# Performance work log

Hardware: AMD Instinct MI355X
Metric: run time of the kernel (lower is better)

The kernel has to match this reference:

```python
import jax, jax.numpy as jnp
import numpy as np

K = 5          # number of spline bins
B = 5.0        # tail bound
HIDDEN = 8
MIN_W = 1e-3; MIN_H = 1e-3; MIN_D = 1e-3  # RQS defaults (Durkan et al.)


def setup_inputs() -> dict:
    n, d = 32768, 64
    L = d - 1
    P = 3 * K - 1
    ks = jax.random.split(jax.random.key(0), 8)
    x = jax.random.normal(ks[0], (n, d), jnp.float32) * 2.0
    init_param = jax.random.uniform(ks[1], (P,), jnp.float32, -0.5, 0.5)
    # ragged first layers: layer l (predicts dim l+1) sees x[:, :l+1]; zero-pad to width L
    mask = (jnp.arange(L)[None, :] <= jnp.arange(L)[:, None]).astype(jnp.float32)
    W1 = jax.random.normal(ks[2], (L, L, HIDDEN), jnp.float32) * 0.2 * mask[:, :, None]
    b1 = jax.random.normal(ks[3], (L, HIDDEN), jnp.float32) * 0.1
    W2 = jax.random.normal(ks[4], (L, HIDDEN, HIDDEN), jnp.float32) * 0.2
    b2 = jax.random.normal(ks[5], (L, HIDDEN), jnp.float32) * 0.1
    W3 = jax.random.normal(ks[6], (L, HIDDEN, P), jnp.float32) * 0.2
    b3 = jax.random.normal(ks[7], (L, P), jnp.float32) * 0.1
    return {"x": x, "init_param": init_param, "W1": W1, "b1": b1,
            "W2": W2, "b2": b2, "W3": W3, "b3": b3}


def _rqs(xf, Wu, Hu, Du):
    # xf: (M,), Wu/Hu: (M,K), Du: (M,K-1) -- vectorized unconstrained RQS, forward
    inside = (xf >= -B) & (xf <= B)
    const = float(np.log(np.exp(1.0 - MIN_D) - 1.0))
    Dpad = jnp.pad(Du, ((0, 0), (1, 1)), constant_values=const)

    widths = MIN_W + (1.0 - MIN_W * K) * jax.nn.softmax(Wu, axis=-1)
    cumw = jnp.pad(jnp.cumsum(widths, -1), ((0, 0), (1, 0)))
    cumw = 2.0 * B * cumw - B
    cumw = cumw.at[:, 0].set(-B).at[:, -1].set(B)
    widths = cumw[:, 1:] - cumw[:, :-1]

    heights = MIN_H + (1.0 - MIN_H * K) * jax.nn.softmax(Hu, axis=-1)
    cumh = jnp.pad(jnp.cumsum(heights, -1), ((0, 0), (1, 0)))
    cumh = 2.0 * B * cumh - B
    cumh = cumh.at[:, 0].set(-B).at[:, -1].set(B)
    heights = cumh[:, 1:] - cumh[:, :-1]

    derivs = MIN_D + jax.nn.softplus(Dpad)  # (M, K+1)

    xc = jnp.clip(xf, -B, B)
    idx = jnp.clip(jnp.sum(xc[:, None] >= cumw, axis=-1) - 1, 0, K - 1)
    take = lambda a: jnp.take_along_axis(a, idx[:, None], axis=-1)[:, 0]

    icw, ibw = take(cumw), take(widths)
    ich, ih = take(cumh), take(heights)
    idl = take(heights / widths)
    idv = take(derivs)
    idvp1 = take(derivs[:, 1:])

    theta = (xc - icw) / ibw
    tmt = theta * (1.0 - theta)
    num = ih * (idl * theta * theta + idv * tmt)
    den = idl + (idv + idvp1 - 2.0 * idl) * tmt
    out = ich + num / den
    dnum = idl * idl * (idvp1 * theta * theta + 2.0 * idl * tmt + idv * (1.0 - theta) ** 2)
    ld = jnp.log(dnum) - 2.0 * jnp.log(den)
    return jnp.where(inside, out, xf), jnp.where(inside, ld, 0.0)


def reference(x, init_param, W1, b1, W2, b2, W3, b3):
    n, d = x.shape
    L = d - 1
    P = 3 * K - 1
    # mask re-applied so padded W1 entries are exactly inert (ragged Linear(i, hidden))
    mask = (jnp.arange(L)[None, :] <= jnp.arange(L)[:, None]).astype(x.dtype)
    h = jnp.tanh(jnp.einsum('nj,ljh->lnh', x[:, :L], W1 * mask[:, :, None]) + b1[:, None, :])
    h = jnp.tanh(jnp.einsum('lnh,lhg->lng', h, W2) + b2[:, None, :])
    out = jnp.einsum('lng,lgp->lnp', h, W3) + b3[:, None, :]      # (L, n, P)
    p0 = jnp.broadcast_to(init_param, (1, n, P))                  # dim 0 uses init_param
    params = jnp.concatenate([p0, out], axis=0).reshape(d * n, P)  # dim-major, matches Ws layout
    Wu, Hu, Du = params[:, :K], params[:, K:2 * K], params[:, 2 * K:]
    xf = x.T.reshape(-1)  # x.transpose(0,1).flatten()
    zs, lds = _rqs(xf, Wu, Hu, Du)
    # NOTE: faithfully replicates the original's reshape of the dim-major flat
    # vector directly to (n, d) (as in the torch source).
    return zs.reshape(n, d), lds.reshape(n, d).sum(axis=1)
```

## Files before the change

### kernel.cpp

```cpp
#include <hip/hip_runtime.h>
#include <hip/hip_bf16.h>
#include <math.h>

#define KK 5
#define Bc 5.0f
#define NN 32768
#define DD 64
#define LL 63
#define PP 14
#define MIN_Wc 0.001f
#define MIN_Hc 0.001f
#define MIN_Dc 0.001f
#define LOG2E 1.44269504088896340736f
#define TWOLOG2E 2.88539008177792681472f
#define LN2 0.69314718055994530942f

typedef float f4 __attribute__((ext_vector_type(4)));
typedef float f32x4 __attribute__((ext_vector_type(4)));
typedef float f2 __attribute__((ext_vector_type(2)));
typedef short short8 __attribute__((ext_vector_type(8)));

__device__ __forceinline__ float rcp_fast(float v)   { return __builtin_amdgcn_rcpf(v); }
__device__ __forceinline__ float exp2_fast(float v)  { return __builtin_amdgcn_exp2f(v); }
__device__ __forceinline__ float log2_fast(float v)  { return __builtin_amdgcn_logf(v); }
__device__ __forceinline__ float tanh_pre(float t2) {
    float e = exp2_fast(t2);
    return 1.0f - 2.0f * rcp_fast(e + 1.0f);
}
__device__ __forceinline__ float softplus2(float v2) {
    return (v2 > 21.7f) ? LN2 * v2 : LN2 * log2_fast(1.0f + exp2_fast(v2));
}
__device__ __forceinline__ ushort to_bf16t(float v) {
    return (ushort)(__float_as_uint(v) >> 16);
}
__device__ __forceinline__ unsigned pack_bf16t2(float v0, float v1) {
    return (__float_as_uint(v0) >> 16) | (__float_as_uint(v1) & 0xFFFF0000u);
}
__device__ __forceinline__ float bflo(unsigned u) { return __uint_as_float(u << 16); }
__device__ __forceinline__ float bfhi(unsigned u) { return __uint_as_float(u & 0xFFFF0000u); }
__device__ __forceinline__ f2 splat2(float v) { f2 r; r.x = v; r.y = v; return r; }
__device__ __forceinline__ f4 splat4(float v) { f4 r; r.x = v; r.y = v; r.z = v; r.w = v; return r; }

__device__ __forceinline__ short8 pack_a(f4 v0, f4 v1) {
    short8 a;
    a[0] = (short)to_bf16t(v0.x); a[1] = (short)to_bf16t(v0.y);
    a[2] = (short)to_bf16t(v0.z); a[3] = (short)to_bf16t(v0.w);
    a[4] = (short)to_bf16t(v1.x); a[5] = (short)to_bf16t(v1.y);
    a[6] = (short)to_bf16t(v1.z); a[7] = (short)to_bf16t(v1.w);
    return a;
}

#define WSL 216
#define H1S 72
#define BS  72

__device__ __forceinline__ void do_dim2(
    int dd, const float* wp, float xf0, float xf1, uint4 hv0, uint4 hv1,
    int s0, int lane, int bx,
    const float* __restrict__ ip, float* __restrict__ out)
{
    float h0_0 = bflo(hv0.x), h1_0 = bflo(hv1.x);
    float h0_1 = bfhi(hv0.x), h1_1 = bfhi(hv1.x);
    float h0_2 = bflo(hv0.y), h1_2 = bflo(hv1.y);
    float h0_3 = bfhi(hv0.y), h1_3 = bfhi(hv1.y);
    float h0_4 = bflo(hv0.z), h1_4 = bflo(hv1.z);
    float h0_5 = bfhi(hv0.z), h1_5 = bfhi(hv1.z);
    float h0_6 = bflo(hv0.w), h1_6 = bflo(hv1.w);
    float h0_7 = bfhi(hv0.w), h1_7 = bfhi(hv1.w);

    f4 a0 = *(const f4*)(wp + 64), b0 = *(const f4*)(wp + 68);
    f4 a1 = a0, b1 = b0;
#define L2STEP(HI, X0, X1) { \
    f4 wa = *(const f4*)(wp + (HI) * 8); \
    f4 wb = *(const f4*)(wp + (HI) * 8 + 4); \
    f4 v0 = splat4(X0), v1 = splat4(X1); \
    a0 += v0 * wa; a1 += v1 * wa; \
    b0 += v0 * wb; b1 += v1 * wb; }
    L2STEP(0, h0_0, h1_0)
    L2STEP(1, h0_1, h1_1)
    L2STEP(2, h0_2, h1_2)
    L2STEP(3, h0_3, h1_3)
    L2STEP(4, h0_4, h1_4)
    L2STEP(5, h0_5, h1_5)
    L2STEP(6, h0_6, h1_6)
    L2STEP(7, h0_7, h1_7)
#undef L2STEP
    float g0_0 = tanh_pre(a0.x), g1_0 = tanh_pre(a1.x);
    float g0_1 = tanh_pre(a0.y), g1_1 = tanh_pre(a1.y);
    float g0_2 = tanh_pre(a0.z), g1_2 = tanh_pre(a1.z);
    float g0_3 = tanh_pre(a0.w), g1_3 = tanh_pre(a1.w);
    float g0_4 = tanh_pre(b0.x), g1_4 = tanh_pre(b1.x);
    float g0_5 = tanh_pre(b0.y), g1_5 = tanh_pre(b1.y);
    float g0_6 = tanh_pre(b0.z), g1_6 = tanh_pre(b1.z);
    float g0_7 = tanh_pre(b0.w), g1_7 = tanh_pre(b1.w);

    f4 pa0 = *(const f4*)(wp + 200), pb0 = *(const f4*)(wp + 204);
    f4 pc0 = *(const f4*)(wp + 208), pd0 = *(const f4*)(wp + 212);
    f4 pa1 = pa0, pb1 = pb0, pc1 = pc0, pd1 = pd0;
#define L3STEP(GI, X0, X1) { \
    const float* wr = wp + 72 + (GI) * 16; \
    f4 w0 = *(const f4*)(wr); \
    f4 w1 = *(const f4*)(wr + 4); \
    f4 w2 = *(const f4*)(wr + 8); \
    f4 w3 = *(const f4*)(wr + 12); \
    f4 v0 = splat4(X0), v1 = splat4(X1); \
    pa0 += v0 * w0; pa1 += v1 * w0; \
    pb0 += v0 * w1; pb1 += v1 * w1; \
    pc0 += v0 * w2; pc1 += v1 * w2; \
    pd0 += v0 * w3; pd1 += v1 * w3; }
    L3STEP(0, g0_0, g1_0)
    L3STEP(1, g0_1, g1_1)
    L3STEP(2, g0_2, g1_2)
    L3STEP(3, g0_3, g1_3)
    L3STEP(4, g0_4, g1_4)
    L3STEP(5, g0_5, g1_5)
    L3STEP(6, g0_6, g1_6)
    L3STEP(7, g0_7, g1_7)
#undef L3STEP

    float p0_0 = pa0.x, p0_1 = pa0.y, p0_2 = pa0.z, p0_3 = pa0.w;
    float p0_4 = pb0.x, p0_5 = pb0.y, p0_6 = pb0.z, p0_7 = pb0.w;
    float p0_8 = pc0.x, p0_9 = pc0.y, p0_10 = pc0.z, p0_11 = pc0.w;
    float p0_12 = pd0.x, p0_13 = pd0.y;
    float p1_0 = pa1.x, p1_1 = pa1.y, p1_2 = pa1.z, p1_3 = pa1.w;
    float p1_4 = pb1.x, p1_5 = pb1.y, p1_6 = pb1.z, p1_7 = pb1.w;
    float p1_8 = pc1.x, p1_9 = pc1.y, p1_10 = pc1.z, p1_11 = pc1.w;
    float p1_12 = pd1.x, p1_13 = pd1.y;

    if (dd == 0) {
        p0_0 = LOG2E * ip[0];  p0_1 = LOG2E * ip[1];  p0_2 = LOG2E * ip[2];
        p0_3 = LOG2E * ip[3];  p0_4 = LOG2E * ip[4];  p0_5 = LOG2E * ip[5];
        p0_6 = LOG2E * ip[6];  p0_7 = LOG2E * ip[7];  p0_8 = LOG2E * ip[8];
        p0_9 = LOG2E * ip[9];  p0_10 = LOG2E * ip[10]; p0_11 = LOG2E * ip[11];
        p0_12 = LOG2E * ip[12]; p0_13 = LOG2E * ip[13];
        p1_0 = p0_0;  p1_1 = p0_1;  p1_2 = p0_2;  p1_3 = p0_3;
        p1_4 = p0_4;  p1_5 = p0_5;  p1_6 = p0_6;  p1_7 = p0_7;
        p1_8 = p0_8;  p1_9 = p0_9;  p1_10 = p0_10; p1_11 = p0_11;
        p1_12 = p0_12; p1_13 = p0_13;
    }

    f4 e0, e1, e2, e3, e4;
    e0.x = exp2_fast(p0_0); e0.y = exp2_fast(p0_5); e0.z = exp2_fast(p1_0); e0.w = exp2_fast(p1_5);
    e1.x = exp2_fast(p0_1); e1.y = exp2_fast(p0_6); e1.z = exp2_fast(p1_1); e1.w = exp2_fast(p1_6);
    e2.x = exp2_fast(p0_2); e2.y = exp2_fast(p0_7); e2.z = exp2_fast(p1_2); e2.w = exp2_fast(p1_7);
    e3.x = exp2_fast(p0_3); e3.y = exp2_fast(p0_8); e3.z = exp2_fast(p1_3); e3.w = exp2_fast(p1_8);
    e4.x = exp2_fast(p0_4); e4.y = exp2_fast(p0_9); e4.z = exp2_fast(p1_4); e4.w = exp2_fast(p1_9);
    f4 es = (e0 + e1) + (e2 + e3) + e4;
    f4 nrm;
    nrm.x = 0.995f * rcp_fast(es.x); nrm.y = 0.995f * rcp_fast(es.y);
    nrm.z = 0.995f * rcp_fast(es.z); nrm.w = 0.995f * rcp_fast(es.w);

    const f4 minv = {MIN_Wc, MIN_Hc, MIN_Wc, MIN_Hc};
    f4 acc4 = splat4(0.f);
    acc4 += minv + nrm * e0;  f4 cb1 = splat4(2.f * Bc) * acc4 - splat4(Bc);
    acc4 += minv + nrm * e1;  f4 cb2 = splat4(2.f * Bc) * acc4 - splat4(Bc);
    acc4 += minv + nrm * e2;  f4 cb3 = splat4(2.f * Bc) * acc4 - splat4(Bc);
    acc4 += minv + nrm * e3;  f4 cb4 = splat4(2.f * Bc) * acc4 - splat4(Bc);

    const float xc0 = fminf(fmaxf(xf0, -Bc), Bc);
    const float xc1 = fminf(fmaxf(xf1, -Bc), Bc);

    float icw0 = -Bc, ich0 = -Bc, hw0 = cb1.x, hh0 = cb1.y;
    float icw1 = -Bc, ich1 = -Bc, hw1 = cb1.z, hh1 = cb1.w;
    float rv0 = p0_10, rvp0 = p0_10, rv1 = p1_10, rvp1 = p1_10;
    bool vone0 = true, vpone0 = false, vone1 = true, vpone1 = false;
    {
        bool c0 = xc0 >= cb1.x;               bool c1 = xc1 >= cb1.z;
        icw0 = c0 ? cb1.x : icw0;             icw1 = c1 ? cb1.z : icw1;
        ich0 = c0 ? cb1.y : ich0;             ich1 = c1 ? cb1.w : ich1;
        hw0  = c0 ? cb2.x : hw0;              hw1  = c1 ? cb2.z : hw1;
        hh0  = c0 ? cb2.y : hh0;              hh1  = c1 ? cb2.w : hh1;
        vone0 = c0 ? false : vone0;           vone1 = c1 ? false : vone1;
        rv0  = c0 ? p0_10 : rv0;              rv1  = c1 ? p1_10 : rv1;
        rvp0 = c0 ? p0_11 : rvp0;             rvp1 = c1 ? p1_11 : rvp1;
    }
    {
        bool c0 = xc0 >= cb2.x;               bool c1 = xc1 >= cb2.z;
        icw0 = c0 ? cb2.x : icw0;             icw1 = c1 ? cb2.z : icw1;
        ich0 = c0 ? cb2.y : ich0;             ich1 = c1 ? cb2.w : ich1;
        hw0  = c0 ? cb3.x : hw0;              hw1  = c1 ? cb3.z : hw1;
        hh0  = c0 ? cb3.y : hh0;              hh1  = c1 ? cb3.w : hh1;
        rv0  = c0 ? p0_11 : rv0;              rv1  = c1 ? p1_11 : rv1;
        rvp0 = c0 ? p0_12 : rvp0;             rvp1 = c1 ? p1_12 : rvp1;
    }
    {
        bool c0 = xc0 >= cb3.x;               bool c1 = xc1 >= cb3.z;
        icw0 = c0 ? cb3.x : icw0;             icw1 = c1 ? cb3.z : icw1;
        ich0 = c0 ? cb3.y : ich0;             ich1 = c1 ? cb3.w : ich1;
        hw0  = c0 ? cb4.x : hw0;              hw1  = c1 ? cb4.z : hw1;
        hh0  = c0 ? cb4.y : hh0;              hh1  = c1 ? cb4.w : hh1;
        rv0  = c0 ? p0_12 : rv0;              rv1  = c1 ? p1_12 : rv1;
        rvp0 = c0 ? p0_13 : rvp0;             rvp1 = c1 ? p1_13 : rvp1;
    }
    {
        bool c0 = xc0 >= cb4.x;               bool c1 = xc1 >= cb4.z;
        icw0 = c0 ? cb4.x : icw0;             icw1 = c1 ? cb4.z : icw1;
        ich0 = c0 ? cb4.y : ich0;             ich1 = c1 ? cb4.w : ich1;
        hw0  = c0 ? Bc : hw0;                 hw1  = c1 ? Bc : hw1;
        hh0  = c0 ? Bc : hh0;                 hh1  = c1 ? Bc : hh1;
        rv0  = c0 ? p0_13 : rv0;              rv1  = c1 ? p1_13 : rv1;
        vpone0 = c0;                          vpone1 = c1;
    }
    const float ibw0 = hw0 - icw0, ih0 = hh0 - ich0;
    const float ibw1 = hw1 - icw1, ih1 = hh1 - ich1;
    const float idv0   = vone0  ? 1.0f : MIN_Dc + softplus2(rv0);
    const float idv1   = vone1  ? 1.0f : MIN_Dc + softplus2(rv1);
    const float idvp0  = vpone0 ? 1.0f : MIN_Dc + softplus2(rvp0);
    const float idvp1_ = vpone1 ? 1.0f : MIN_Dc + softplus2(rvp1);

    const float ibr0 = rcp_fast(ibw0);        const float ibr1 = rcp_fast(ibw1);
    const float idl0 = ih0 * ibr0;            const float idl1 = ih1 * ibr1;
    const float th0 = (xc0 - icw0) * ibr0;    const float th1 = (xc1 - icw1) * ibr1;
    const float om0 = 1.0f - th0;             const float om1 = 1.0f - th1;
    const float tm0 = th0 * om0;              const float tm1 = th1 * om1;
    const float num0 = ih0 * (idl0 * th0 * th0 + idv0 * tm0);
    const float num1 = ih1 * (idl1 * th1 * th1 + idv1 * tm1);
    const float den0 = idl0 + (idv0 + idvp0 - 2.0f * idl0) * tm0;
    const float den1 = idl1 + (idv1 + idvp1_ - 2.0f * idl1) * tm1;
    const float dr0 = rcp_fast(den0);         const float dr1 = rcp_fast(den1);
    const float out0 = ich0 + num0 * dr0;     const float out1v = ich1 + num1 * dr1;
    const float dn0 = idl0 * idl0 * (idvp0 * th0 * th0 + 2.0f * idl0 * tm0 + idv0 * om0 * om0);
    const float dn1 = idl1 * idl1 * (idvp1_ * th1 * th1 + 2.0f * idl1 * tm1 + idv1 * om1 * om1);
    const float ld0 = LN2 * log2_fast(dn0 * dr0 * dr0);
    const float ld1 = LN2 * log2_fast(dn1 * dr1 * dr1);

    const bool in0 = (xf0 >= -Bc) && (xf0 <= Bc);
    const bool in1 = (xf1 >= -Bc) && (xf1 <= Bc);
    const float z0 = in0 ? out0 : xf0;        const float z1 = in1 ? out1v : xf1;
    float lv0 = in0 ? ld0 : 0.0f;             float lv1 = in1 ? ld1 : 0.0f;

    out[dd * NN + s0 + lane] = z0;
    out[dd * NN + s0 + 64 + lane] = z1;

    #pragma unroll
    for (int off = 32; off > 0; off >>= 1) {
        lv0 += __shfl_down(lv0, off);
        lv1 += __shfl_down(lv1, off);
    }
    if (lane == 0) {
        out[NN * DD + dd * (NN / 64) + 2 * bx]     = lv0;
        out[NN * DD + dd * (NN / 64) + 2 * bx + 1] = lv1;
    }
}

__global__ __launch_bounds__(256, 4) void fused_kernel(
    const float* __restrict__ x, const float* __restrict__ init_param,
    const float* __restrict__ W1, const float* __restrict__ b1,
    const float* __restrict__ W2, const float* __restrict__ b2,
    const float* __restrict__ W3, const float* __restrict__ b3,
    float* __restrict__ out)
{
    __shared__ ushort h1c[128 * H1S];
    __shared__ float  wl[8 * WSL];
    __shared__ ushort Blds[64 * BS];
    const int tid = threadIdx.x;
    const int s0 = blockIdx.x * 128;
    const int y  = blockIdx.y;
    const int bx = blockIdx.x;
    const int lane = tid & 63;
    const int wave = __builtin_amdgcn_readfirstlane(tid >> 6);
    const int ln = lane & 15, qg = lane >> 4;
    const int l0 = y * 8;

    const int dA = y * 8 + 1 + 2 * wave;
    const int dB = (y == 7 && wave == 3) ? 0 : dA + 1;
    const float* xr0 = x + (size_t)(s0 + lane) * 64;
    const float* xr1 = xr0 + 64 * 64;
    float xA0 = xr0[dA], xA1 = xr1[dA];
    float xB0 = xr0[dB], xB1 = xr1[dB];

    short8 a0_0, a1_0, a0_1, a1_1;
    {
        const float* p0 = x + (size_t)(s0 + wave * 16 + ln) * 64 + qg * 8;
        const float* p1 = p0 + 64 * 64;
        a0_0 = pack_a(*(const f4*)p0, *(const f4*)(p0 + 4));
        a0_1 = pack_a(*(const f4*)p1, *(const f4*)(p1 + 4));
        if (y >= 4) {
            a1_0 = pack_a(*(const f4*)(p0 + 32), *(const f4*)(p0 + 36));
            a1_1 = pack_a(*(const f4*)(p1 + 32), *(const f4*)(p1 + 36));
        } else { a1_0 = a0_0; a1_1 = a0_1; }
    }

    {
        const int n_local = tid >> 2;
        const int n = y * 64 + n_local;
        const int l = n >> 3, h = n & 7;
        const float* src = W1 + (size_t)l * 63 * 8 + h;
        unsigned* drow = (unsigned*)&Blds[n_local * BS];
        if (y < 4) {
            const int kc0 = (tid & 3) * 8;
            #pragma unroll
            for (int j = 0; j < 4; ++j) {
                int k = kc0 + 2 * j;
                float v0 = src[(size_t)k * 8];
                float v1 = src[(size_t)(k + 1) * 8];
                drow[(kc0 >> 1) + j] = pack_bf16t2(v0, v1);
            }
        } else {
            const int kc0 = (tid & 3) * 16;
            #pragma unroll
            for (int j = 0; j < 8; ++j) {
                int k = kc0 + 2 * j;
                float v0 = (n < 504 && k < 63)     ? src[(size_t)k * 8]       : 0.f;
                float v1 = (n < 504 && k + 1 < 63) ? src[(size_t)(k + 1) * 8] : 0.f;
                drow[(kc0 >> 1) + j] = pack_bf16t2(v0, v1);
            }
        }
    }

    if (tid < 128) {
        int s = tid >> 4, o = (tid & 15) * 4;
        if (l0 + s < LL)
            *(f4*)&wl[s * WSL + o] = splat4(TWOLOG2E) * (*(const f4*)&W2[(l0 + s) * 64 + o]);
    }
    if (tid < 64) {
        int s = tid >> 3, o = tid & 7;
        if (l0 + s < LL) wl[s * WSL + 64 + o] = TWOLOG2E * b2[(l0 + s) * 8 + o];
    }
    #pragma unroll
    for (int q0 = 0; q0 < 448; q0 += 256) {
        int q = q0 + tid;
        if (q < 448) {
            int s = q / 56, r = q % 56, g = r / 7, o = r % 7;
            if (l0 + s < LL)
                *(f2*)&wl[s * WSL + 72 + g * 16 + o * 2] =
                    splat2(LOG2E) * (*(const f2*)&W3[(l0 + s) * 112 + g * 14 + o * 2]);
        }
    }
    if (tid < 64) {
        int s = tid >> 3, g = tid & 7;
        *(f2*)&wl[s * WSL + 72 + g * 16 + 14] = splat2(0.f);
    }
    if (tid < 112) {
        int s = tid / 14, o = tid % 14;
        wl[s * WSL + 200 + o] = LOG2E * b3[(l0 + s < LL ? l0 + s : 0) * PP + o];
    }
    if (tid < 16) {
        int s = tid >> 1, o = 214 + (tid & 1);
        wl[s * WSL + o] = 0.f;
    }
    __syncthreads();

    #pragma unroll
    for (int nt = 0; nt < 4; ++nt) {
        int ncol = y * 64 + nt * 16 + ln;
        const ushort* brow = &Blds[(nt * 16 + ln) * BS + qg * 8];
        short8 bf0 = *(const short8*)brow;
        f32x4 acc0 = {0.f, 0.f, 0.f, 0.f};
        f32x4 acc1 = {0.f, 0.f, 0.f, 0.f};
        acc0 = __builtin_amdgcn_mfma_f32_16x16x32_bf16(a0_0, bf0, acc0, 0, 0, 0);
        acc1 = __builtin_amdgcn_mfma_f32_16x16x32_bf16(a0_1, bf0, acc1, 0, 0, 0);
        if (y >= 4) {
            short8 bf1 = *(const short8*)(brow + 32);
            acc0 = __builtin_amdgcn_mfma_f32_16x16x32_bf16(a1_0, bf1, acc0, 0, 0, 0);
            acc1 = __builtin_amdgcn_mfma_f32_16x16x32_bf16(a1_1, bf1, acc1, 0, 0, 0);
        }
        float bias2 = (ncol < 504) ? TWOLOG2E * b1[ncol] : 0.f;
        #pragma unroll
        for (int r = 0; r < 4; ++r) {
            int row = wave * 16 + qg * 4 + r;
            float v0 = tanh_pre(fmaf(TWOLOG2E, acc0[r], bias2));
            float v1 = tanh_pre(fmaf(TWOLOG2E, acc1[r], bias2));
            h1c[row * H1S + nt * 16 + ln] = to_bf16t(v0);
            h1c[(row + 64) * H1S + nt * 16 + ln] = to_bf16t(v1);
        }
    }
    __syncthreads();

    const int slA = 2 * wave, slB = 2 * wave + 1;
    uint4 hA0 = *(const uint4*)&h1c[lane * H1S + slA * 8];
    uint4 hA1 = *(const uint4*)&h1c[(lane + 64) * H1S + slA * 8];
    uint4 hB0 = *(const uint4*)&h1c[lane * H1S + slB * 8];
    uint4 hB1 = *(const uint4*)&h1c[(lane + 64) * H1S + slB * 8];

    do_dim2(dA, wl + slA * WSL, xA0, xA1, hA0, hA1, s0, lane, bx, init_param, out);
    do_dim2(dB, wl + slB * WSL, xB0, xB1, hB0, hB1, s0, lane, bx, init_param, out);
}

extern "C" void kernel_launch(void* const* d_in, const int* in_sizes, int n_in,
                              void* d_out, int out_size, void* d_ws, size_t ws_size,
                              hipStream_t stream) {
    const float* x          = (const float*)d_in[0];
    const float* init_param = (const float*)d_in[1];
    const float* W1         = (const float*)d_in[2];
    const float* b1         = (const float*)d_in[3];
    const float* W2         = (const float*)d_in[4];
    const float* b2         = (const float*)d_in[5];
    const float* W3         = (const float*)d_in[6];
    const float* b3         = (const float*)d_in[7];
    float* out = (float*)d_out;

    fused_kernel<<<dim3(256, 8), 256, 0, stream>>>(x, init_param, W1, b1,
                                                   W2, b2, W3, b3, out);
}
```

Measured before the change: 104.6 us.

## Prepack W1 to bf16 in a workspace kernel, read B fragments from global

Adds a small pre-kernel that converts the ragged W1 weights into a packed bf16 B-matrix layout in workspace once per call. The main kernel then loads MFMA B fragments straight from that global buffer instead of having every block gather, convert and stage W1 into shared memory. This drops the Blds buffer and one barrier, so LDS use per block is lower. It costs an extra kernel launch and uncoalesced-ish global fragment reads that rely on L2 hits. A fallback to the old LDS path stays for when no workspace is given.

```diff
diff --git a/kernel.cpp b/kernel.cpp
--- a/kernel.cpp
+++ b/kernel.cpp
@@ -53,6 +53,7 @@
 #define WSL 216
 #define H1S 72
 #define BS  72
+
 
 __device__ __forceinline__ void do_dim2(
     int dd, const float* wp, float xf0, float xf1, uint4 hv0, uint4 hv1,
@@ -243,7 +244,134 @@
     }
 }
 
+__device__ __forceinline__ void stage_wl(
+    int tid, int l0, float* wl,
+    const float* __restrict__ W2, const float* __restrict__ b2,
+    const float* __restrict__ W3, const float* __restrict__ b3)
+{
+    if (tid < 128) {
+        int s = tid >> 4, o = (tid & 15) * 4;
+        if (l0 + s < LL)
+            *(f4*)&wl[s * WSL + o] = splat4(TWOLOG2E) * (*(const f4*)&W2[(l0 + s) * 64 + o]);
+    }
+    if (tid < 64) {
+        int s = tid >> 3, o = tid & 7;
+        if (l0 + s < LL) wl[s * WSL + 64 + o] = TWOLOG2E * b2[(l0 + s) * 8 + o];
+    }
+    #pragma unroll
+    for (int q0 = 0; q0 < 448; q0 += 256) {
+        int q = q0 + tid;
+        if (q < 448) {
+            int s = q / 56, r = q % 56, g = r / 7, o = r % 7;
+            if (l0 + s < LL)
+                *(f2*)&wl[s * WSL + 72 + g * 16 + o * 2] =
+                    splat2(LOG2E) * (*(const f2*)&W3[(l0 + s) * 112 + g * 14 + o * 2]);
+        }
+    }
+    if (tid < 64) {
+        int s = tid >> 3, g = tid & 7;
+        *(f2*)&wl[s * WSL + 72 + g * 16 + 14] = splat2(0.f);
+    }
+    if (tid < 112) {
+        int s = tid / 14, o = tid % 14;
+        wl[s * WSL + 200 + o] = LOG2E * b3[(l0 + s < LL ? l0 + s : 0) * PP + o];
+    }
+    if (tid < 16) {
+        int s = tid >> 1, o = 214 + (tid & 1);
+        wl[s * WSL + o] = 0.f;
+    }
+}
+
+__global__ __launch_bounds__(256) void pack_b1(
+    const float* __restrict__ W1, unsigned* __restrict__ Bp)
+{
+    int id = blockIdx.x * 256 + threadIdx.x;
+    int n = id >> 5;
+    int kw = id & 31;
+    int l = n >> 3, h = n & 7;
+    const float* src = W1 + (size_t)l * 63 * 8 + h;
+    int k0 = 2 * kw, k1 = k0 + 1;
+    float v0 = (n < 504 && k0 < 63) ? src[(size_t)k0 * 8] : 0.f;
+    float v1 = (n < 504 && k1 < 63) ? src[(size_t)k1 * 8] : 0.f;
+    Bp[id] = pack_bf16t2(v0, v1);
+}
+
 __global__ __launch_bounds__(256, 4) void fused_kernel(
+    const float* __restrict__ x, const float* __restrict__ init_param,
+    const ushort* __restrict__ Bp, const float* __restrict__ b1,
+    const float* __restrict__ W2, const float* __restrict__ b2,
+    const float* __restrict__ W3, const float* __restrict__ b3,
+    float* __restrict__ out)
+{
+    __shared__ ushort h1c[128 * H1S];
+    __shared__ float  wl[8 * WSL];
+    const int tid = threadIdx.x;
+    const int s0 = blockIdx.x * 128;
+    const int y  = blockIdx.y;
+    const int bx = blockIdx.x;
+    const int lane = tid & 63;
+    const int wave = __builtin_amdgcn_readfirstlane(tid >> 6);
+    const int ln = lane & 15, qg = lane >> 4;
+    const int l0 = y * 8;
+
+    const int dA = y * 8 + 1 + 2 * wave;
+    const int dB = (y == 7 && wave == 3) ? 0 : dA + 1;
+    const float* xr0 = x + (size_t)(s0 + lane) * 64;
+    const float* xr1 = xr0 + 64 * 64;
+    float xA0 = xr0[dA], xA1 = xr1[dA];
+    float xB0 = xr0[dB], xB1 = xr1[dB];
+
+    short8 a0_0, a1_0, a0_1, a1_1;
+    {
+        const float* p0 = x + (size_t)(s0 + wave * 16 + ln) * 64 + qg * 8;
+        const float* p1 = p0 + 64 * 64;
+        a0_0 = pack_a(*(const f4*)p0, *(const f4*)(p0 + 4));
+        a0_1 = pack_a(*(const f4*)p1, *(const f4*)(p1 + 4));
+        if (y >= 4) {
+            a1_0 = pack_a(*(const f4*)(p0 + 32), *(const f4*)(p0 + 36));
+            a1_1 = pack_a(*(const f4*)(p1 + 32), *(const f4*)(p1 + 36));
+        } else { a1_0 = a0_0; a1_1 = a0_1; }
+    }
+
+    stage_wl(tid, l0, wl, W2, b2, W3, b3);
+
+    #pragma unroll 2
+    for (int nt = 0; nt < 4; ++nt) {
+        int ncol = y * 64 + nt * 16 + ln;
+        const ushort* brow = Bp + (size_t)ncol * 64 + qg * 8;
+        short8 bf0 = *(const short8*)brow;
+        f32x4 acc0 = {0.f, 0.f, 0.f, 0.f};
+        f32x4 acc1 = {0.f, 0.f, 0.f, 0.f};
+        acc0 = __builtin_amdgcn_mfma_f32_16x16x32_bf16(a0_0, bf0, acc0, 0, 0, 0);
+        acc1 = __builtin_amdgcn_mfma_f32_16x16x32_bf16(a0_1, bf0, acc1, 0, 0, 0);
+        if (y >= 4) {
+            short8 bf1 = *(const short8*)(brow + 32);
+            acc0 = __builtin_amdgcn_mfma_f32_16x16x32_bf16(a1_0, bf1, acc0, 0, 0, 0);
+            acc1 = __builtin_amdgcn_mfma_f32_16x16x32_bf16(a1_1, bf1, acc1, 0, 0, 0);
+        }
+        float bias2 = (ncol < 504) ? TWOLOG2E * b1[ncol] : 0.f;
+        #pragma unroll
+        for (int r = 0; r < 4; ++r) {
+            int row = wave * 16 + qg * 4 + r;
+            float v0 = tanh_pre(fmaf(TWOLOG2E, acc0[r], bias2));
+            float v1 = tanh_pre(fmaf(TWOLOG2E, acc1[r], bias2));
+            h1c[row * H1S + nt * 16 + ln] = to_bf16t(v0);
+            h1c[(row + 64) * H1S + nt * 16 + ln] = to_bf16t(v1);
+        }
+    }
+    __syncthreads();
+
+    const int slA = 2 * wave, slB = 2 * wave + 1;
+    uint4 hA0 = *(const uint4*)&h1c[lane * H1S + slA * 8];
+    uint4 hA1 = *(const uint4*)&h1c[(lane + 64) * H1S + slA * 8];
+    uint4 hB0 = *(const uint4*)&h1c[lane * H1S + slB * 8];
+    uint4 hB1 = *(const uint4*)&h1c[(lane + 64) * H1S + slB * 8];
+
+    do_dim2(dA, wl + slA * WSL, xA0, xA1, hA0, hA1, s0, lane, bx, init_param, out);
+    do_dim2(dB, wl + slB * WSL, xB0, xB1, hB0, hB1, s0, lane, bx, init_param, out);
+}
+
+__global__ __launch_bounds__(256, 4) void fused_kernel_lds(
     const float* __restrict__ x, const float* __restrict__ init_param,
     const float* __restrict__ W1, const float* __restrict__ b1,
     const float* __restrict__ W2, const float* __restrict__ b2,
@@ -308,37 +436,7 @@
         }
     }
 
-    if (tid < 128) {
-        int s = tid >> 4, o = (tid & 15) * 4;
-        if (l0 + s < LL)
-            *(f4*)&wl[s * WSL + o] = splat4(TWOLOG2E) * (*(const f4*)&W2[(l0 + s) * 64 + o]);
-    }
-    if (tid < 64) {
-        int s = tid >> 3, o = tid & 7;
-        if (l0 + s < LL) wl[s * WSL + 64 + o] = TWOLOG2E * b2[(l0 + s) * 8 + o];
-    }
-    #pragma unroll
-    for (int q0 = 0; q0 < 448; q0 += 256) {
-        int q = q0 + tid;
-        if (q < 448) {
-            int s = q / 56, r = q % 56, g = r / 7, o = r % 7;
-            if (l0 + s < LL)
-                *(f2*)&wl[s * WSL + 72 + g * 16 + o * 2] =
-                    splat2(LOG2E) * (*(const f2*)&W3[(l0 + s) * 112 + g * 14 + o * 2]);
-        }
-    }
-    if (tid < 64) {
-        int s = tid >> 3, g = tid & 7;
-        *(f2*)&wl[s * WSL + 72 + g * 16 + 14] = splat2(0.f);
-    }
-    if (tid < 112) {
-        int s = tid / 14, o = tid % 14;
-        wl[s * WSL + 200 + o] = LOG2E * b3[(l0 + s < LL ? l0 + s : 0) * PP + o];
-    }
-    if (tid < 16) {
-        int s = tid >> 1, o = 214 + (tid & 1);
-        wl[s * WSL + o] = 0.f;
-    }
+    stage_wl(tid, l0, wl, W2, b2, W3, b3);
     __syncthreads();
 
     #pragma unroll
@@ -390,6 +488,14 @@
     const float* b3         = (const float*)d_in[7];
     float* out = (float*)d_out;
 
-    fused_kernel<<<dim3(256, 8), 256, 0, stream>>>(x, init_param, W1, b1,
-                                                   W2, b2, W3, b3, out);
-}
+    if (d_ws != nullptr && ws_size >= 512 * 64 * sizeof(ushort)) {
+        unsigned* Bp = (unsigned*)d_ws;
+        pack_b1<<<64, 256, 0, stream>>>(W1, Bp);
+        fused_kernel<<<dim3(256, 8), 256, 0, stream>>>(x, init_param,
+                                                       (const ushort*)Bp, b1,
+                                                       W2, b2, W3, b3, out);
+    } else {
+        fused_kernel_lds<<<dim3(256, 8), 256, 0, stream>>>(x, init_param, W1, b1,
+                                                           W2, b2, W3, b3, out);
+    }
+}
```

After: 105.7 us. About the same (+1.0%).
